# Kernel optimization log

Measured on AMD Instinct MI355X. Metric: run time of the kernel, lower is better.

## Reference

```python
import jax, jax.numpy as jnp
import numpy as np

N_NODES = 20000
N_EDGES = 320000
NFEAT = 50
ALPHA = 0.2  # leaky relu slope
EPS = 1e-16


def _gat_head(x, src, dst, W, a, concat):
    # x: (N, Fin), W: (Fin, Fout), a: (2*Fout,)
    N = x.shape[0]
    Wh = x @ W                      # (N, Fout)
    Fout = W.shape[1]
    # edge_h @ a == Wh[src] @ a[:Fout] + Wh[dst] @ a[Fout:]
    s_src = Wh @ a[:Fout]           # (N,)
    s_dst = Wh @ a[Fout:]           # (N,)
    e = jax.nn.leaky_relu(s_src[src] + s_dst[dst], negative_slope=ALPHA)  # (E,)
    # segment softmax over incoming edges of each target node
    e_max = jax.ops.segment_max(e, dst, num_segments=N)   # (N,)
    e_exp = jnp.exp(e - e_max[dst])                         # (E,)
    e_sum = jax.ops.segment_sum(e_exp, dst, num_segments=N)
    att = e_exp / (e_sum[dst] + EPS)                        # (E,)
    msg = Wh[src] * att[:, None]                            # (E, Fout)
    h = jax.ops.segment_sum(msg, dst, num_segments=N)       # (N, Fout)
    return jax.nn.elu(h) if concat else h


def _multi_head(x, src, dst, W, a, concat):
    # W: (H, Fin, Fout), a: (H, 2*Fout) -> (H, N, Fout)
    return jax.vmap(_gat_head, in_axes=(None, None, None, 0, 0, None))(x, src, dst, W, a, concat)


def setup_inputs() -> dict:
    key = jax.random.key(0)
    ks = jax.random.split(key, 8)
    x = jax.random.normal(ks[0], (N_NODES, NFEAT), dtype=jnp.float32)
    edge_index = jax.random.randint(ks[1], (2, N_EDGES), 0, N_NODES, dtype=jnp.int64)
    s = 0.1
    W1 = jax.random.normal(ks[2], (4, NFEAT, 256), dtype=jnp.float32) * s
    a1 = jax.random.normal(ks[3], (4, 512), dtype=jnp.float32) * s
    W2 = jax.random.normal(ks[4], (4, 1024, 256), dtype=jnp.float32) * s
    a2 = jax.random.normal(ks[5], (4, 512), dtype=jnp.float32) * s
    W3 = jax.random.normal(ks[6], (6, 1024, 121), dtype=jnp.float32) * s
    a3 = jax.random.normal(ks[7], (6, 242), dtype=jnp.float32) * s
    return {"x": x, "edge_index": edge_index, "W1": W1, "a1": a1, "W2": W2, "a2": a2, "W3": W3, "a3": a3}


def reference(x, edge_index, W1, a1, W2, a2, W3, a3):
    src, dst = edge_index[0], edge_index[1]
    N = x.shape[0]
    # layer 1: 4 heads, concat -> (N, 1024), then elu
    h1 = _multi_head(x, src, dst, W1, a1, True)      # (4, N, 256)
    x1 = jnp.transpose(h1, (1, 0, 2)).reshape(N, -1)  # concat along feature dim
    x1 = jax.nn.elu(x1)
    # layer 2: 4 heads, concat + skip connection, then elu
    h2 = _multi_head(x1, src, dst, W2, a2, True)
    x2 = jnp.transpose(h2, (1, 0, 2)).reshape(N, -1)
    x2 = jax.nn.elu(x2 + x1)
    # layer 3: 6 heads, no concat-elu, mean over heads
    h3 = _multi_head(x2, src, dst, W3, a3, False)     # (6, N, 121)
    x3 = jnp.mean(h3, axis=0)
    return jax.nn.sigmoid(x3)
```

## Files before the change

kernel.cpp:

```cpp
#include <hip/hip_runtime.h>
#include <cstdint>

#define N_NODES 20000
#define N_EDGES 320000
#define ALPHA 0.2f
#define GAT_EPS 1e-16f
#define MPAD 20096
#define RBLK 157
#define RHI 20
#define SCAN_BLKS 80
#define BT_ROWS 1152

typedef __attribute__((ext_vector_type(8))) _Float16 half8;
typedef __attribute__((ext_vector_type(4))) _Float16 half4t;
typedef __attribute__((ext_vector_type(16))) float f32x16;
typedef __attribute__((ext_vector_type(2))) float f32x2;

__device__ __forceinline__ float elu1(float x) { return x > 0.f ? x : __expf(x) - 1.f; }

__device__ __forceinline__ unsigned char f2fp8(float x) {
    return (unsigned char)(__builtin_amdgcn_cvt_pk_fp8_f32(x, 0.f, 0, false) & 0xff);
}

__device__ __forceinline__ void async16(const void* g, void* l) {
    __builtin_amdgcn_global_load_lds(
        (const __attribute__((address_space(1))) unsigned int*)g,
        (__attribute__((address_space(3))) unsigned int*)l, 16, 0, 0);
}

__device__ __forceinline__ float rdlanef(float v, int j) {
    return __int_as_float(__builtin_amdgcn_readlane(__float_as_int(v), j));
}

__global__ void hist_kernel(const int* __restrict__ dst, int* __restrict__ counts, int E) {
    int e = blockIdx.x * blockDim.x + threadIdx.x;
    if (e < E) atomicAdd(&counts[dst[e]], 1);
}

__global__ void scan1_kernel(const int* __restrict__ counts, int* __restrict__ excl,
                             int* __restrict__ partial, int N) {
    __shared__ int sh[256];
    int t = threadIdx.x, b = blockIdx.x;
    int i = b * 256 + t;
    int v = (i < N) ? counts[i] : 0;
    sh[t] = v;
    __syncthreads();
    for (int d = 1; d < 256; d <<= 1) {
        int x = (t >= d) ? sh[t - d] : 0;
        __syncthreads();
        sh[t] += x;
        __syncthreads();
    }
    if (i < N) excl[i] = sh[t] - v;
    if (t == 255) partial[b] = sh[255];
}

__global__ void scan2_kernel(int* __restrict__ partial) {
    __shared__ int sh[128];
    int t = threadIdx.x;
    int v = (t < SCAN_BLKS) ? partial[t] : 0;
    sh[t] = v;
    __syncthreads();
    for (int d = 1; d < 128; d <<= 1) {
        int x = (t >= d) ? sh[t - d] : 0;
        __syncthreads();
        sh[t] += x;
        __syncthreads();
    }
    if (t < SCAN_BLKS) partial[t] = sh[t] - v;
}

__global__ void scan3_kernel(const int* __restrict__ excl, const int* __restrict__ partial,
                             int* __restrict__ rowptr, int* __restrict__ cursor, int N, int E) {
    int t = threadIdx.x, b = blockIdx.x;
    int i = b * 256 + t;
    if (i < N) {
        int v = excl[i] + partial[b];
        rowptr[i] = v;
        cursor[i] = v;
    }
    if (i == 0) rowptr[N] = E;
}

__global__ void scatter_kernel(const int* __restrict__ src, const int* __restrict__ dst,
                               int* __restrict__ cursor, int* __restrict__ esrc, int E) {
    int e = blockIdx.x * blockDim.x + threadIdx.x;
    if (e < E) {
        int p = atomicAdd(&cursor[dst[e]], 1);
        esrc[p] = src[e];
    }
}

__global__ void pack_x16(const float* __restrict__ x, _Float16* __restrict__ A) {
    int idx = blockIdx.x * 256 + threadIdx.x;
    int r = idx >> 6, c = idx & 63;
    float v = (r < N_NODES && c < 50) ? x[r * 50 + c] : 0.f;
    A[idx] = (_Float16)v;
}

__global__ void pack_bt1(const float* __restrict__ W, _Float16* __restrict__ Bt) {
    int idx = blockIdx.x * 256 + threadIdx.x;
    int c = idx >> 6, k = idx & 63;
    int h = c >> 8, f = c & 255;
    float v = (k < 50) ? W[((size_t)h * 50 + k) * 256 + f] : 0.f;
    Bt[idx] = (_Float16)v;
}

__global__ void pack_bt16(const float* __restrict__ W, _Float16* __restrict__ Bt,
                          int F, int Fpad, int Ctot) {
    int c = blockIdx.y;
    int k = blockIdx.x * blockDim.x + threadIdx.x;
    float v = 0.f;
    if (c < Ctot) {
        int h = c / Fpad, f = c - h * Fpad;
        if (f < F) v = W[(size_t)h * 1024 * F + (size_t)k * F + f];
    }
    Bt[(size_t)c * 1024 + k] = (_Float16)v;
}

__global__ __launch_bounds__(64) void wtilde_kernel(const float* __restrict__ W,
                                                    const float* __restrict__ a,
                                                    _Float16* __restrict__ BT, int Kreal,
                                                    int Kdim, int F, int H, int Nfeat) {
    int k = blockIdx.x, j = blockIdx.y;
    if (j >= 2 * H) return;
    int lane = threadIdx.x;
    int h = j < H ? j : j - H;
    int ao = j < H ? 0 : F;
    float s = 0.f;
    if (k < Kreal) {
        const float* wp = W + ((size_t)h * Kreal + k) * F;
        const float* ap = a + (size_t)h * 2 * F + ao;
        for (int f = lane; f < F; f += 64) s += wp[f] * ap[f];
    }
#pragma unroll
    for (int off = 32; off; off >>= 1) s += __shfl_down(s, off);
    if (lane == 0) BT[(size_t)(Nfeat + j) * Kdim + k] = (_Float16)s;
}

__global__ __launch_bounds__(256) void gemm_f16(const _Float16* __restrict__ A,
                                                const _Float16* __restrict__ BT,
                                                unsigned char* __restrict__ C8,
                                                float* __restrict__ SPRE,
                                                int M, int Nfeat, int ld, int Kdim, int Cblk) {
    int id = blockIdx.x;
    int xm = id & 7, q = id >> 3;
    int cb = q % Cblk, rh = q / Cblk;
    int rb = rh * 8 + xm;
    if (rb >= RBLK) return;
    __shared__ __align__(16) _Float16 sA[2][128 * 64];
    __shared__ __align__(16) _Float16 sB[2][128 * 64];
    int t = threadIdx.x;
    int row0 = rb * 128, col0 = cb * 128;
    int lane = t & 63, wave = t >> 6;
    int wm = wave >> 1, wn = wave & 1;
    int l31 = lane & 31;
    int lhi = lane >> 5;

    const _Float16* gA = A + (size_t)row0 * Kdim;
    const _Float16* gB = BT + (size_t)col0 * Kdim;

    int sR[4], sgl[4];
#pragma unroll
    for (int i = 0; i < 4; i++) {
        int m = i * 256 + t;
        sR[i] = m >> 3;
        sgl[i] = (m & 7) ^ (sR[i] & 7);
    }

    f32x16 acc[2][2] = {};

#pragma unroll
    for (int i = 0; i < 4; i++) {
        const _Float16* pa = gA + (size_t)sR[i] * Kdim + sgl[i] * 8;
        const _Float16* pb = gB + (size_t)sR[i] * Kdim + sgl[i] * 8;
        async16(pa, &sA[0][(i * 256 + t) * 8]);
        async16(pb, &sB[0][(i * 256 + t) * 8]);
    }

    int cur = 0;
    for (int k0 = 0; k0 < Kdim; k0 += 64) {
        __syncthreads();
        int nxt = k0 + 64;
        if (nxt < Kdim) {
            int nb = cur ^ 1;
#pragma unroll
            for (int i = 0; i < 4; i++) {
                const _Float16* pa = gA + (size_t)sR[i] * Kdim + nxt + sgl[i] * 8;
                const _Float16* pb = gB + (size_t)sR[i] * Kdim + nxt + sgl[i] * 8;
                async16(pa, &sA[nb][(i * 256 + t) * 8]);
                async16(pb, &sB[nb][(i * 256 + t) * 8]);
            }
        }
        const _Float16* cA = sA[cur];
        const _Float16* cB = sB[cur];
#pragma unroll
        for (int kk = 0; kk < 4; kk++) {
            int g = kk * 2 + lhi;
            half8 af[2], bf[2];
#pragma unroll
            for (int mt = 0; mt < 2; mt++) {
                int R = wm * 64 + mt * 32 + l31;
                int gp = g ^ (R & 7);
                af[mt] = *(const half8*)(cA + R * 64 + gp * 8);
            }
#pragma unroll
            for (int nt = 0; nt < 2; nt++) {
                int R = wn * 64 + nt * 32 + l31;
                int gp = g ^ (R & 7);
                bf[nt] = *(const half8*)(cB + R * 64 + gp * 8);
            }
#pragma unroll
            for (int mt = 0; mt < 2; mt++)
#pragma unroll
                for (int nt = 0; nt < 2; nt++)
                    acc[mt][nt] = __builtin_amdgcn_mfma_f32_32x32x16_f16(af[mt], bf[nt], acc[mt][nt], 0, 0, 0);
        }
        cur ^= 1;
    }

    int cb32 = col0 + wn * 64 + l31;
    int rb32 = row0 + wm * 64 + 4 * lhi;
#pragma unroll
    for (int mt = 0; mt < 2; mt++)
#pragma unroll
        for (int nt = 0; nt < 2; nt++) {
            int gc = cb32 + nt * 32;
            if (gc < Nfeat) {
#pragma unroll
                for (int r = 0; r < 16; r++) {
                    int gr = rb32 + mt * 32 + (r & 3) + 8 * (r >> 2);
                    if (gr < M) C8[(size_t)gr * ld + gc] = f2fp8(acc[mt][nt][r]);
                }
            } else if (gc < Nfeat + 12) {
                int j = gc - Nfeat;
#pragma unroll
                for (int r = 0; r < 16; r++) {
                    int gr = rb32 + mt * 32 + (r & 3) + 8 * (r >> 2);
                    if (gr < M) SPRE[(size_t)j * N_NODES + gr] = acc[mt][nt][r];
                }
            }
        }
}

__global__ __launch_bounds__(256) void attagg256_kernel(const int* __restrict__ rowptr,
                                                        const int* __restrict__ esrc,
                                                        const float* __restrict__ SPRE,
                                                        const unsigned char* __restrict__ WH8,
                                                        _Float16* __restrict__ X16,
                                                        int use_skip, int N) {
    int n = blockIdx.x;
    int h = threadIdx.x >> 6;
    int lane = threadIdx.x & 63;
    int start = rowptr[n], end = rowptr[n + 1];
    int cnt = end - start;
    const float* ss = SPRE + (size_t)h * N;
    float sd = SPRE[(size_t)(4 + h) * N + n];
    const unsigned char* Wb = WH8 + h * 256 + lane * 4;
    float a0 = 0.f, a1 = 0.f, a2 = 0.f, a3 = 0.f;

    if (cnt <= 64) {
        int e = start + lane;
        bool act = e < end;
        int idx = act ? esrc[e] : 0;

        unsigned int wA[8], wB[8], wC[8];
        auto ISSUE = [&](unsigned int (&buf)[8], int base) {
#pragma unroll
            for (int u = 0; u < 8; u++) {
                int ij = __builtin_amdgcn_readlane(idx, base + u);
                buf[u] = *(const unsigned int*)(Wb + ((size_t)(unsigned)ij << 10));
            }
        };
        ISSUE(wA, 0);
        if (cnt > 8) ISSUE(wB, 8);
        if (cnt > 16) ISSUE(wC, 16);

        float sc = -1e30f;
        if (act) {
            sc = ss[idx] + sd;
            sc = sc > 0.f ? sc : ALPHA * sc;
        }
        float m = sc;
#pragma unroll
        for (int off = 1; off < 64; off <<= 1) m = fmaxf(m, __shfl_xor(m, off));
        float ptil = act ? __expf(sc - m) : 0.f;
        float s = ptil;
#pragma unroll
        for (int off = 1; off < 64; off <<= 1) s += __shfl_xor(s, off);
        float p = ptil * (1.f / (s + GAT_EPS));

        auto CONSUME = [&](unsigned int (&buf)[8], int base) {
#pragma unroll
            for (int u = 0; u < 8; u++) {
                float pj = rdlanef(p, base + u);
                f32x2 lo = __builtin_amdgcn_cvt_pk_f32_fp8((int)buf[u], false);
                f32x2 hi = __builtin_amdgcn_cvt_pk_f32_fp8((int)buf[u], true);
                a0 += pj * lo.x; a1 += pj * lo.y; a2 += pj * hi.x; a3 += pj * hi.y;
            }
        };
        CONSUME(wA, 0);
        if (cnt > 8)  { if (cnt > 24) ISSUE(wA, 24); CONSUME(wB, 8); }
        if (cnt > 16) { if (cnt > 32) ISSUE(wB, 32); CONSUME(wC, 16); }
        if (cnt > 24) { if (cnt > 40) ISSUE(wC, 40); CONSUME(wA, 24); }
        if (cnt > 32) { if (cnt > 48) ISSUE(wA, 48); CONSUME(wB, 32); }
        if (cnt > 40) { if (cnt > 56) ISSUE(wB, 56); CONSUME(wC, 40); }
        if (cnt > 48) CONSUME(wA, 48);
        if (cnt > 56) CONSUME(wB, 56);
    } else {
        float m = -1e30f, s = 0.f;
        int sidx = 0; float ssc = -1e30f;
        for (int e0 = start; e0 < end; e0 += 64) {
            int e = e0 + lane;
            bool act = e < end;
            int idx = act ? esrc[e] : 0;
            float sc = -1e30f;
            if (act) {
                sc = ss[idx] + sd;
                sc = sc > 0.f ? sc : ALPHA * sc;
            }
            sidx = idx; ssc = sc;
            float mn = fmaxf(m, sc);
            s = s * __expf(m - mn) + (act ? __expf(sc - mn) : 0.f);
            m = mn;
        }
        float lm = m;
#pragma unroll
        for (int off = 1; off < 64; off <<= 1) m = fmaxf(m, __shfl_xor(m, off));
        float ptil = s * __expf(lm - m);
        s = ptil;
#pragma unroll
        for (int off = 1; off < 64; off <<= 1) s += __shfl_xor(s, off);
        float inv = 1.f / (s + GAT_EPS);

        int lastStart = start + (((end - start - 1) >> 6) << 6);
        for (int e0 = start; e0 < end; e0 += 64) {
            int e = e0 + lane;
            bool act = e < end;
            int idx; float p;
            if (e0 == lastStart) {
                idx = sidx;
                p = act ? __expf(ssc - m) * inv : 0.f;
            } else {
                idx = act ? esrc[e] : 0;
                float sc = -1e30f;
                if (act) {
                    sc = ss[idx] + sd;
                    sc = sc > 0.f ? sc : ALPHA * sc;
                }
                p = act ? __expf(sc - m) * inv : 0.f;
            }
            int cn = end - e0; if (cn > 64) cn = 64;
            int j = 0;
            for (; j + 4 <= cn; j += 4) {
                int i0 = __builtin_amdgcn_readlane(idx, j);
                int i1 = __builtin_amdgcn_readlane(idx, j + 1);
                int i2 = __builtin_amdgcn_readlane(idx, j + 2);
                int i3 = __builtin_amdgcn_readlane(idx, j + 3);
                float p0 = rdlanef(p, j), p1 = rdlanef(p, j + 1);
                float p2 = rdlanef(p, j + 2), p3 = rdlanef(p, j + 3);
                unsigned int w0 = *(const unsigned int*)(Wb + (size_t)i0 * 1024);
                unsigned int w1 = *(const unsigned int*)(Wb + (size_t)i1 * 1024);
                unsigned int w2 = *(const unsigned int*)(Wb + (size_t)i2 * 1024);
                unsigned int w3 = *(const unsigned int*)(Wb + (size_t)i3 * 1024);
                f32x2 l0 = __builtin_amdgcn_cvt_pk_f32_fp8((int)w0, false);
                f32x2 h0v = __builtin_amdgcn_cvt_pk_f32_fp8((int)w0, true);
                f32x2 l1 = __builtin_amdgcn_cvt_pk_f32_fp8((int)w1, false);
                f32x2 h1v = __builtin_amdgcn_cvt_pk_f32_fp8((int)w1, true);
                f32x2 l2 = __builtin_amdgcn_cvt_pk_f32_fp8((int)w2, false);
                f32x2 h2v = __builtin_amdgcn_cvt_pk_f32_fp8((int)w2, true);
                f32x2 l3 = __builtin_amdgcn_cvt_pk_f32_fp8((int)w3, false);
                f32x2 h3v = __builtin_amdgcn_cvt_pk_f32_fp8((int)w3, true);
                a0 += p0 * l0.x + p1 * l1.x + p2 * l2.x + p3 * l3.x;
                a1 += p0 * l0.y + p1 * l1.y + p2 * l2.y + p3 * l3.y;
                a2 += p0 * h0v.x + p1 * h1v.x + p2 * h2v.x + p3 * h3v.x;
                a3 += p0 * h0v.y + p1 * h1v.y + p2 * h2v.y + p3 * h3v.y;
            }
            for (; j < cn; j++) {
                int ij = __builtin_amdgcn_readlane(idx, j);
                float pj = rdlanef(p, j);
                unsigned int w = *(const unsigned int*)(Wb + (size_t)ij * 1024);
                f32x2 lo = __builtin_amdgcn_cvt_pk_f32_fp8((int)w, false);
                f32x2 hi = __builtin_amdgcn_cvt_pk_f32_fp8((int)w, true);
                a0 += pj * lo.x; a1 += pj * lo.y; a2 += pj * hi.x; a3 += pj * hi.y;
            }
        }
    }

    size_t o = (size_t)n * 1024 + h * 256 + lane * 4;
    float v0, v1, v2, v3;
    if (use_skip) {
        half4t sk = *(const half4t*)(X16 + o);
        v0 = elu1(elu1(a0) + (float)sk.x);
        v1 = elu1(elu1(a1) + (float)sk.y);
        v2 = elu1(elu1(a2) + (float)sk.z);
        v3 = elu1(elu1(a3) + (float)sk.w);
    } else {
        v0 = elu1(elu1(a0)); v1 = elu1(elu1(a1));
        v2 = elu1(elu1(a2)); v3 = elu1(elu1(a3));
    }
    half4t r;
    r.x = (_Float16)v0; r.y = (_Float16)v1; r.z = (_Float16)v2; r.w = (_Float16)v3;
    *(half4t*)(X16 + o) = r;
}

__global__ __launch_bounds__(384) void attagg726_kernel(const int* __restrict__ rowptr,
                                                        const int* __restrict__ esrc,
                                                        const float* __restrict__ SPRE,
                                                        const unsigned char* __restrict__ WH8,
                                                        float* __restrict__ out, int N) {
    __shared__ float part[6][124];
    int n = blockIdx.x;
    int t = threadIdx.x;
    int h = t >> 6;
    int lane = t & 63;
    int start = rowptr[n], end = rowptr[n + 1];
    int cnt = end - start;
    const float* ss = SPRE + (size_t)h * N;
    float sd = SPRE[(size_t)(6 + h) * N + n];
    const unsigned char* Wb = WH8 + h * 124 + 2 * lane;
    float a0 = 0.f, a1 = 0.f;

    if (cnt <= 64) {
        int e = start + lane;
        bool act = e < end;
        int idx = act ? esrc[e] : 0;

        unsigned short wA[8], wB[8], wC[8];
        auto ISSUE = [&](unsigned short (&buf)[8], int base) {
#pragma unroll
            for (int u = 0; u < 8; u++) {
                int ij = __builtin_amdgcn_readlane(idx, base + u);
                buf[u] = *(const unsigned short*)(Wb + (size_t)(unsigned)ij * 768u);
            }
        };
        ISSUE(wA, 0);
        if (cnt > 8) ISSUE(wB, 8);
        if (cnt > 16) ISSUE(wC, 16);

        float sc = -1e30f;
        if (act) {
            sc = ss[idx] + sd;
            sc = sc > 0.f ? sc : ALPHA * sc;
        }
        float m = sc;
#pragma unroll
        for (int off = 1; off < 64; off <<= 1) m = fmaxf(m, __shfl_xor(m, off));
        float ptil = act ? __expf(sc - m) : 0.f;
        float s = ptil;
#pragma unroll
        for (int off = 1; off < 64; off <<= 1) s += __shfl_xor(s, off);
        float p = ptil * (1.f / (s + GAT_EPS));

        auto CONSUME = [&](unsigned short (&buf)[8], int base) {
#pragma unroll
            for (int u = 0; u < 8; u++) {
                float pj = rdlanef(p, base + u);
                f32x2 f = __builtin_amdgcn_cvt_pk_f32_fp8((int)buf[u], false);
                a0 += pj * f.x; a1 += pj * f.y;
            }
        };
        CONSUME(wA, 0);
        if (cnt > 8)  { if (cnt > 24) ISSUE(wA, 24); CONSUME(wB, 8); }
        if (cnt > 16) { if (cnt > 32) ISSUE(wB, 32); CONSUME(wC, 16); }
        if (cnt > 24) { if (cnt > 40) ISSUE(wC, 40); CONSUME(wA, 24); }
        if (cnt > 32) { if (cnt > 48) ISSUE(wA, 48); CONSUME(wB, 32); }
        if (cnt > 40) { if (cnt > 56) ISSUE(wB, 56); CONSUME(wC, 40); }
        if (cnt > 48) CONSUME(wA, 48);
        if (cnt > 56) CONSUME(wB, 56);
    } else {
        float m = -1e30f, s = 0.f;
        int sidx = 0; float ssc = -1e30f;
        for (int e0 = start; e0 < end; e0 += 64) {
            int e = e0 + lane;
            bool act = e < end;
            int idx = act ? esrc[e] : 0;
            float sc = -1e30f;
            if (act) {
                sc = ss[idx] + sd;
                sc = sc > 0.f ? sc : ALPHA * sc;
            }
            sidx = idx; ssc = sc;
            float mn = fmaxf(m, sc);
            s = s * __expf(m - mn) + (act ? __expf(sc - mn) : 0.f);
            m = mn;
        }
        float lm = m;
#pragma unroll
        for (int off = 1; off < 64; off <<= 1) m = fmaxf(m, __shfl_xor(m, off));
        float ptil = s * __expf(lm - m);
        s = ptil;
#pragma unroll
        for (int off = 1; off < 64; off <<= 1) s += __shfl_xor(s, off);
        float inv = 1.f / (s + GAT_EPS);

        int lastStart = start + (((end - start - 1) >> 6) << 6);
        for (int e0 = start; e0 < end; e0 += 64) {
            int e = e0 + lane;
            bool act = e < end;
            int idx; float p;
            if (e0 == lastStart) {
                idx = sidx;
                p = act ? __expf(ssc - m) * inv : 0.f;
            } else {
                idx = act ? esrc[e] : 0;
                float sc = -1e30f;
                if (act) {
                    sc = ss[idx] + sd;
                    sc = sc > 0.f ? sc : ALPHA * sc;
                }
                p = act ? __expf(sc - m) * inv : 0.f;
            }
            int cn = end - e0; if (cn > 64) cn = 64;
            int j = 0;
            for (; j + 4 <= cn; j += 4) {
                int i0 = __builtin_amdgcn_readlane(idx, j);
                int i1 = __builtin_amdgcn_readlane(idx, j + 1);
                int i2 = __builtin_amdgcn_readlane(idx, j + 2);
                int i3 = __builtin_amdgcn_readlane(idx, j + 3);
                float p0 = rdlanef(p, j), p1 = rdlanef(p, j + 1);
                float p2 = rdlanef(p, j + 2), p3 = rdlanef(p, j + 3);
                unsigned short w0 = *(const unsigned short*)(Wb + (size_t)i0 * 768);
                unsigned short w1 = *(const unsigned short*)(Wb + (size_t)i1 * 768);
                unsigned short w2 = *(const unsigned short*)(Wb + (size_t)i2 * 768);
                unsigned short w3 = *(const unsigned short*)(Wb + (size_t)i3 * 768);
                f32x2 f0 = __builtin_amdgcn_cvt_pk_f32_fp8((int)w0, false);
                f32x2 f1 = __builtin_amdgcn_cvt_pk_f32_fp8((int)w1, false);
                f32x2 f2 = __builtin_amdgcn_cvt_pk_f32_fp8((int)w2, false);
                f32x2 f3 = __builtin_amdgcn_cvt_pk_f32_fp8((int)w3, false);
                a0 += p0 * f0.x + p1 * f1.x + p2 * f2.x + p3 * f3.x;
                a1 += p0 * f0.y + p1 * f1.y + p2 * f2.y + p3 * f3.y;
            }
            for (; j < cn; j++) {
                int ij = __builtin_amdgcn_readlane(idx, j);
                float pj = rdlanef(p, j);
                unsigned short w = *(const unsigned short*)(Wb + (size_t)ij * 768);
                f32x2 f = __builtin_amdgcn_cvt_pk_f32_fp8((int)w, false);
                a0 += pj * f.x; a1 += pj * f.y;
            }
        }
    }

    if (lane < 62) {
        part[h][2 * lane]     = a0;
        part[h][2 * lane + 1] = a1;
    }
    __syncthreads();
    if (t < 121) {
        float tot = (part[0][t] + part[1][t] + part[2][t] +
                     part[3][t] + part[4][t] + part[5][t]) * (1.f / 6.f);
        out[(size_t)n * 121 + t] = 1.f / (1.f + __expf(-tot));
    }
}

extern "C" void kernel_launch(void* const* d_in, const int* in_sizes, int n_in,
                              void* d_out, int out_size, void* d_ws, size_t ws_size,
                              hipStream_t stream) {
    const float* x  = (const float*)d_in[0];
    const int*   ei = (const int*)d_in[1];
    const float* W1 = (const float*)d_in[2];
    const float* a1 = (const float*)d_in[3];
    const float* W2 = (const float*)d_in[4];
    const float* a2 = (const float*)d_in[5];
    const float* W3 = (const float*)d_in[6];
    const float* a3 = (const float*)d_in[7];
    float* out = (float*)d_out;
    const int N = N_NODES, E = N_EDGES;
    const int* src = ei;
    const int* dst = ei + E;

    char* ws = (char*)d_ws;
    size_t off = 0;
    auto alloc = [&](size_t b) { size_t o = off; off += (b + 255) & ~(size_t)255; return o; };
    _Float16* X16  = (_Float16*)(ws + alloc((size_t)MPAD * 1024 * 2));
    unsigned char* WH8 = (unsigned char*)(ws + alloc((size_t)MPAD * 1024));
    _Float16* BT16 = (_Float16*)(ws + alloc((size_t)BT_ROWS * 1024 * 2));
    _Float16* A1   = (_Float16*)(ws + alloc((size_t)MPAD * 64 * 2));
    _Float16* BT1  = (_Float16*)(ws + alloc((size_t)BT_ROWS * 64 * 2));
    float* SPRE   = (float*)(ws + alloc((size_t)12 * N * 4));
    int*   rowptr = (int*)(ws + alloc((size_t)(N + 1) * 4));
    int*   cursor = (int*)(ws + alloc((size_t)N * 4));
    int*   counts = (int*)(ws + alloc((size_t)N * 4));
    int*   excl   = (int*)(ws + alloc((size_t)N * 4));
    int*   partial= (int*)(ws + alloc((size_t)SCAN_BLKS * 4));
    int*   esrc   = (int*)(ws + alloc((size_t)E * 4));

    hipMemsetAsync(counts, 0, (size_t)N * 4, stream);
    hist_kernel<<<(E + 255) / 256, 256, 0, stream>>>(dst, counts, E);
    scan1_kernel<<<SCAN_BLKS, 256, 0, stream>>>(counts, excl, partial, N);
    scan2_kernel<<<1, 128, 0, stream>>>(partial);
    scan3_kernel<<<SCAN_BLKS, 256, 0, stream>>>(excl, partial, rowptr, cursor, N, E);
    scatter_kernel<<<(E + 255) / 256, 256, 0, stream>>>(src, dst, cursor, esrc, E);
    hipMemsetAsync(X16 + (size_t)N * 1024, 0, (size_t)(MPAD - N) * 1024 * 2, stream);

    pack_x16<<<MPAD * 64 / 256, 256, 0, stream>>>(x, A1);
    pack_bt1<<<1024 * 64 / 256, 256, 0, stream>>>(W1, BT1);
    wtilde_kernel<<<dim3(64, 8), 64, 0, stream>>>(W1, a1, BT1, 50, 64, 256, 4, 1024);
    gemm_f16<<<8 * RHI * 9, 256, 0, stream>>>(A1, BT1, WH8, SPRE, N, 1024, 1024, 64, 9);
    attagg256_kernel<<<N, 256, 0, stream>>>(rowptr, esrc, SPRE, WH8, X16, 0, N);

    pack_bt16<<<dim3(4, 1024), 256, 0, stream>>>(W2, BT16, 256, 256, 1024);
    wtilde_kernel<<<dim3(1024, 8), 64, 0, stream>>>(W2, a2, BT16, 1024, 1024, 256, 4, 1024);
    gemm_f16<<<8 * RHI * 9, 256, 0, stream>>>(X16, BT16, WH8, SPRE, N, 1024, 1024, 1024, 9);
    attagg256_kernel<<<N, 256, 0, stream>>>(rowptr, esrc, SPRE, WH8, X16, 1, N);

    pack_bt16<<<dim3(4, 744), 256, 0, stream>>>(W3, BT16, 121, 124, 744);
    wtilde_kernel<<<dim3(1024, 12), 64, 0, stream>>>(W3, a3, BT16, 1024, 1024, 121, 6, 744);
    gemm_f16<<<8 * RHI * 6, 256, 0, stream>>>(X16, BT16, WH8, SPRE, N, 744, 768, 1024, 6);
    attagg726_kernel<<<N, 384, 0, stream>>>(rowptr, esrc, SPRE, WH8, out, N);
}
```

Measured before the change: 448.5 us.

## Single-buffer GEMM LDS and deepen gather prefetch to four buffers

The f16 MFMA GEMM drops its double-buffered LDS prefetch. Each K step now loads the tile, syncs, then computes, which halves LDS use and may raise occupancy but removes the overlap between loads and math. The aggregation kernels for layers 1/2 and layer 3 add a fourth gather buffer, so up to 32 neighbour rows are in flight before consumption begins. This trades extra registers for more memory-level parallelism.

```diff
diff --git a/kernel.cpp b/kernel.cpp
--- a/kernel.cpp
+++ b/kernel.cpp
@@ -148,8 +148,8 @@
     int cb = q % Cblk, rh = q / Cblk;
     int rb = rh * 8 + xm;
     if (rb >= RBLK) return;
-    __shared__ __align__(16) _Float16 sA[2][128 * 64];
-    __shared__ __align__(16) _Float16 sB[2][128 * 64];
+    __shared__ __align__(16) _Float16 sA[128 * 64];
+    __shared__ __align__(16) _Float16 sB[128 * 64];
     int t = threadIdx.x;
     int row0 = rb * 128, col0 = cb * 128;
     int lane = t & 63, wave = t >> 6;
@@ -170,30 +170,16 @@
 
     f32x16 acc[2][2] = {};
 
-#pragma unroll
-    for (int i = 0; i < 4; i++) {
-        const _Float16* pa = gA + (size_t)sR[i] * Kdim + sgl[i] * 8;
-        const _Float16* pb = gB + (size_t)sR[i] * Kdim + sgl[i] * 8;
-        async16(pa, &sA[0][(i * 256 + t) * 8]);
-        async16(pb, &sB[0][(i * 256 + t) * 8]);
-    }
-
-    int cur = 0;
     for (int k0 = 0; k0 < Kdim; k0 += 64) {
         __syncthreads();
-        int nxt = k0 + 64;
-        if (nxt < Kdim) {
-            int nb = cur ^ 1;
-#pragma unroll
-            for (int i = 0; i < 4; i++) {
-                const _Float16* pa = gA + (size_t)sR[i] * Kdim + nxt + sgl[i] * 8;
-                const _Float16* pb = gB + (size_t)sR[i] * Kdim + nxt + sgl[i] * 8;
-                async16(pa, &sA[nb][(i * 256 + t) * 8]);
-                async16(pb, &sB[nb][(i * 256 + t) * 8]);
-            }
-        }
-        const _Float16* cA = sA[cur];
-        const _Float16* cB = sB[cur];
+#pragma unroll
+        for (int i = 0; i < 4; i++) {
+            const _Float16* pa = gA + (size_t)sR[i] * Kdim + k0 + sgl[i] * 8;
+            const _Float16* pb = gB + (size_t)sR[i] * Kdim + k0 + sgl[i] * 8;
+            async16(pa, sA + (i * 256 + t) * 8);
+            async16(pb, sB + (i * 256 + t) * 8);
+        }
+        __syncthreads();
 #pragma unroll
         for (int kk = 0; kk < 4; kk++) {
             int g = kk * 2 + lhi;
@@ -202,13 +188,13 @@
             for (int mt = 0; mt < 2; mt++) {
                 int R = wm * 64 + mt * 32 + l31;
                 int gp = g ^ (R & 7);
-                af[mt] = *(const half8*)(cA + R * 64 + gp * 8);
+                af[mt] = *(const half8*)(sA + R * 64 + gp * 8);
             }
 #pragma unroll
             for (int nt = 0; nt < 2; nt++) {
                 int R = wn * 64 + nt * 32 + l31;
                 int gp = g ^ (R & 7);
-                bf[nt] = *(const half8*)(cB + R * 64 + gp * 8);
+                bf[nt] = *(const half8*)(sB + R * 64 + gp * 8);
             }
 #pragma unroll
             for (int mt = 0; mt < 2; mt++)
@@ -216,7 +202,6 @@
                 for (int nt = 0; nt < 2; nt++)
                     acc[mt][nt] = __builtin_amdgcn_mfma_f32_32x32x16_f16(af[mt], bf[nt], acc[mt][nt], 0, 0, 0);
         }
-        cur ^= 1;
     }
 
     int cb32 = col0 + wn * 64 + l31;
@@ -264,7 +249,7 @@
         bool act = e < end;
         int idx = act ? esrc[e] : 0;
 
-        unsigned int wA[8], wB[8], wC[8];
+        unsigned int wA[8], wB[8], wC[8], wD[8];
         auto ISSUE = [&](unsigned int (&buf)[8], int base) {
 #pragma unroll
             for (int u = 0; u < 8; u++) {
@@ -273,8 +258,9 @@
             }
         };
         ISSUE(wA, 0);
-        if (cnt > 8) ISSUE(wB, 8);
+        if (cnt > 8)  ISSUE(wB, 8);
         if (cnt > 16) ISSUE(wC, 16);
+        if (cnt > 24) ISSUE(wD, 24);
 
         float sc = -1e30f;
         if (act) {
@@ -300,13 +286,13 @@
             }
         };
         CONSUME(wA, 0);
-        if (cnt > 8)  { if (cnt > 24) ISSUE(wA, 24); CONSUME(wB, 8); }
-        if (cnt > 16) { if (cnt > 32) ISSUE(wB, 32); CONSUME(wC, 16); }
-        if (cnt > 24) { if (cnt > 40) ISSUE(wC, 40); CONSUME(wA, 24); }
-        if (cnt > 32) { if (cnt > 48) ISSUE(wA, 48); CONSUME(wB, 32); }
-        if (cnt > 40) { if (cnt > 56) ISSUE(wB, 56); CONSUME(wC, 40); }
-        if (cnt > 48) CONSUME(wA, 48);
-        if (cnt > 56) CONSUME(wB, 56);
+        if (cnt > 8)  { if (cnt > 32) ISSUE(wA, 32); CONSUME(wB, 8); }
+        if (cnt > 16) { if (cnt > 40) ISSUE(wB, 40); CONSUME(wC, 16); }
+        if (cnt > 24) { if (cnt > 48) ISSUE(wC, 48); CONSUME(wD, 24); }
+        if (cnt > 32) { if (cnt > 56) ISSUE(wD, 56); CONSUME(wA, 32); }
+        if (cnt > 40) CONSUME(wB, 40);
+        if (cnt > 48) CONSUME(wC, 48);
+        if (cnt > 56) CONSUME(wD, 56);
     } else {
         float m = -1e30f, s = 0.f;
         int sidx = 0; float ssc = -1e30f;
@@ -426,7 +412,7 @@
         bool act = e < end;
         int idx = act ? esrc[e] : 0;
 
-        unsigned short wA[8], wB[8], wC[8];
+        unsigned short wA[8], wB[8], wC[8], wD[8];
         auto ISSUE = [&](unsigned short (&buf)[8], int base) {
 #pragma unroll
             for (int u = 0; u < 8; u++) {
@@ -435,8 +421,9 @@
             }
         };
         ISSUE(wA, 0);
-        if (cnt > 8) ISSUE(wB, 8);
+        if (cnt > 8)  ISSUE(wB, 8);
         if (cnt > 16) ISSUE(wC, 16);
+        if (cnt > 24) ISSUE(wD, 24);
 
         float sc = -1e30f;
         if (act) {
@@ -461,13 +448,13 @@
             }
         };
         CONSUME(wA, 0);
-        if (cnt > 8)  { if (cnt > 24) ISSUE(wA, 24); CONSUME(wB, 8); }
-        if (cnt > 16) { if (cnt > 32) ISSUE(wB, 32); CONSUME(wC, 16); }
-        if (cnt > 24) { if (cnt > 40) ISSUE(wC, 40); CONSUME(wA, 24); }
-        if (cnt > 32) { if (cnt > 48) ISSUE(wA, 48); CONSUME(wB, 32); }
-        if (cnt > 40) { if (cnt > 56) ISSUE(wB, 56); CONSUME(wC, 40); }
-        if (cnt > 48) CONSUME(wA, 48);
-        if (cnt > 56) CONSUME(wB, 56);
+        if (cnt > 8)  { if (cnt > 32) ISSUE(wA, 32); CONSUME(wB, 8); }
+        if (cnt > 16) { if (cnt > 40) ISSUE(wB, 40); CONSUME(wC, 16); }
+        if (cnt > 24) { if (cnt > 48) ISSUE(wC, 48); CONSUME(wD, 24); }
+        if (cnt > 32) { if (cnt > 56) ISSUE(wD, 56); CONSUME(wA, 32); }
+        if (cnt > 40) CONSUME(wB, 40);
+        if (cnt > 48) CONSUME(wC, 48);
+        if (cnt > 56) CONSUME(wD, 56);
     } else {
         float m = -1e30f, s = 0.f;
         int sidx = 0; float ssc = -1e30f;
```

After: 444.5 us. No clear change (-0.9%).
